# Kernel tuning notes

Measured on AMD Instinct MI355X. Metric: run time of the kernel, lower is better.

The kernel has to match this reference:

```python
import jax, jax.numpy as jnp
import numpy as np
from jax import lax

KERNEL_EPS = 1e-4   # eps in softmax_kernel
ATTN_EPS = 1e-6     # eps in causal_linear_attention
CHUNK = 64          # chunk length for the causal scan


def softmax_kernel(data, projection_matrix, is_query):
    # data: [b,h,n,d], projection_matrix: [r,d]
    d = data.shape[-1]
    r = projection_matrix.shape[0]
    data_normalizer = d ** -0.25
    ratio = r ** -0.5
    data_dash = jnp.einsum('bhnd,rd->bhnr', data_normalizer * data, projection_matrix)
    diag_data = (jnp.sum(data ** 2, axis=-1) * 0.5 * data_normalizer ** 2)[..., None]  # [b,h,n,1]
    if is_query:
        stab = jnp.max(data_dash, axis=-1, keepdims=True)
    else:
        stab = jnp.max(data_dash)
    return ratio * (jnp.exp(data_dash - diag_data - stab) + KERNEL_EPS)


def causal_linear_attention(qp, kp, v, chunk=CHUNK, eps=ATTN_EPS):
    # qp,kp: [b,h,n,r] feature maps; v: [b,h,n,e]
    b, h, n, r = qp.shape
    e = v.shape[-1]
    nc = n // chunk
    # -> [nc, b, h, chunk, *] for lax.scan over chunks
    qs = jnp.moveaxis(qp.reshape(b, h, nc, chunk, r), 2, 0)
    ks = jnp.moveaxis(kp.reshape(b, h, nc, chunk, r), 2, 0)
    vs = jnp.moveaxis(v.reshape(b, h, nc, chunk, e), 2, 0)

    def step(carry, xs):
        k_last, ctx_last = carry  # [b,h,r], [b,h,r,e]
        qch, kch, vch = xs        # [b,h,c,r], [b,h,c,r], [b,h,c,e]
        k_cum = k_last[:, :, None, :] + jnp.cumsum(kch, axis=2)              # [b,h,c,r]
        D_inv = 1.0 / jnp.einsum('bhcr,bhcr->bhc', qch, k_cum + eps)         # [b,h,c]
        ctx = jnp.einsum('bhcr,bhce->bhcre', kch, vch)                       # [b,h,c,r,e]
        ctx_cum = ctx_last[:, :, None] + jnp.cumsum(ctx, axis=2)             # [b,h,c,r,e]
        out = jnp.einsum('bhcre,bhcr,bhc->bhce', ctx_cum, qch, D_inv)        # [b,h,c,e]
        return (k_cum[:, :, -1], ctx_cum[:, :, -1]), out

    init = (jnp.zeros((b, h, r), qp.dtype), jnp.zeros((b, h, r, e), qp.dtype))
    _, outs = lax.scan(step, init, (qs, ks, vs))  # outs: [nc,b,h,c,e]
    return jnp.moveaxis(outs, 0, 2).reshape(b, h, n, e)


def setup_inputs() -> dict:
    key = jax.random.key(0)
    kq, kk, kv, kp = jax.random.split(key, 4)
    b, h, n, d, r = 2, 8, 4096, 64, 256
    q = jax.random.normal(kq, (b, h, n, d), dtype=jnp.float32)
    k = jax.random.normal(kk, (b, h, n, d), dtype=jnp.float32)
    v = jax.random.normal(kv, (b, h, n, d), dtype=jnp.float32)
    projection_matrix = jax.random.normal(kp, (r, d), dtype=jnp.float32)
    return {"q": q, "k": k, "v": v, "projection_matrix": projection_matrix}


def reference(q, k, v, projection_matrix):
    qp = softmax_kernel(q, projection_matrix, is_query=True)
    kp = softmax_kernel(k, projection_matrix, is_query=False)
    return causal_linear_attention(qp, kp, v)
```

## Files before the change

kernel.cpp:

```cpp
#include <hip/hip_runtime.h>


typedef unsigned short ushort_t;
typedef __attribute__((ext_vector_type(8))) short bf16x8;
typedef __attribute__((ext_vector_type(4))) float f32x4;

#define KEPS 1e-4f
#define AEPS 1e-6f
#define NORMIZER 0.35355339059327373f
#define RATIO 0.0625f

__device__ __forceinline__ ushort_t bf16r(float f) {
  unsigned u = __float_as_uint(f);
  return (ushort_t)((u + 0x7fffu + ((u >> 16) & 1u)) >> 16);
}
__device__ __forceinline__ float ubf(ushort_t h) {
  return __uint_as_float((unsigned)h << 16);
}
__device__ __forceinline__ unsigned cvtpk(float lo, float hi) {
  unsigned r;
  asm("v_cvt_pk_bf16_f32 %0, %1, %2" : "=v"(r) : "v"(lo), "v"(hi));
  return r;
}
union U32V { unsigned u[4]; bf16x8 v; };

__global__ __launch_bounds__(256) void pconv_kernel(
    const float* __restrict__ P, ushort_t* __restrict__ Phi,
    ushort_t* __restrict__ Plo)
{
  int idx = blockIdx.x * 1024 + threadIdx.x;
  #pragma unroll
  for (int p = 0; p < 4; ++p) {
    int i = idx + p * 256;
    float x = P[i];
    ushort_t h = bf16r(x);
    Phi[i] = h;
    Plo[i] = bf16r(x - ubf(h));
  }
}

__device__ __forceinline__ void stage_ptile(const ushort_t* __restrict__ gt,
                                            ushort_t* lds0, int tid) {
  int wv = tid >> 6, lane = tid & 63;
  #pragma unroll
  for (int i = 0; i < 2; ++i) {
    int D = i * 256 + wv * 64 + lane;
    int row = D >> 3, c3 = D & 7;
    int sc = (row << 3) | (c3 ^ (row & 7));
    __builtin_amdgcn_global_load_lds(
        (const __attribute__((address_space(1))) void*)(gt + sc * 8),
        (__attribute__((address_space(3))) void*)(lds0 + (i * 256 + wv * 64) * 8),
        16, 0, 0);
  }
}

__global__ __launch_bounds__(256, 4) void feat_mfma(
    const float* __restrict__ Q, const float* __restrict__ K,
    const float* __restrict__ V,
    const ushort_t* __restrict__ Phi, const ushort_t* __restrict__ Plo,
    ushort_t* __restrict__ qp, ushort_t* __restrict__ E,
    float* __restrict__ bmax,
    ushort_t* __restrict__ SE, float* __restrict__ zE,
    float* __restrict__ SV)
{
  __shared__ union {
    struct {
      ushort_t Xhi[64 * 72];
      ushort_t Xlo[64 * 72];
      ushort_t Pt[2][4096];
    } s;
    ushort_t outb[64 * 268];
    ushort_t Et[256 * 72];
  } u;
  __shared__ float diagS[64];
  __shared__ float redm[4];

  int bid = blockIdx.x, tid = threadIdx.x;
  bool isK = bid < 1024;
  int bc = bid;
  const float* X = isK ? K : Q;
  size_t rowbase = (size_t)(isK ? bid : bid - 1024) * 64;

  int lane = tid & 63, wv = tid >> 6;
  int n15 = lane & 15, quad = lane >> 4;

  stage_ptile(Phi, &u.s.Pt[0][0], tid);

  float vraw[16];
  if (isK) {
    #pragma unroll
    for (int ks = 0; ks < 2; ++ks)
      #pragma unroll
      for (int jj = 0; jj < 8; ++jj) {
        int pos = quad * 8 + 32 * ks + jj;
        vraw[ks * 8 + jj] = V[rowbase * 64 + (size_t)pos * 64 + 16 * wv + n15];
      }
  }

  #pragma unroll
  for (int p = 0; p < 4; ++p) {
    int idx = tid + p * 256;
    int row = idx >> 4, c4 = idx & 15;
    float4 x = *(const float4*)&X[(rowbase + row) * 64 + c4 * 4];
    unsigned h0 = cvtpk(x.x, x.y);
    unsigned h1 = cvtpk(x.z, x.w);
    float r0 = x.x - __uint_as_float(h0 << 16);
    float r1 = x.y - __uint_as_float(h0 & 0xffff0000u);
    float r2 = x.z - __uint_as_float(h1 << 16);
    float r3 = x.w - __uint_as_float(h1 & 0xffff0000u);
    unsigned l0 = cvtpk(r0, r1);
    unsigned l1 = cvtpk(r2, r3);
    unsigned* ph = (unsigned*)&u.s.Xhi[row * 72 + c4 * 4];
    ph[0] = h0; ph[1] = h1;
    unsigned* pl = (unsigned*)&u.s.Xlo[row * 72 + c4 * 4];
    pl[0] = l0; pl[1] = l1;
    float ss = x.x * x.x + x.y * x.y + x.z * x.z + x.w * x.w;
    ss += __shfl_xor(ss, 1, 64); ss += __shfl_xor(ss, 2, 64);
    ss += __shfl_xor(ss, 4, 64); ss += __shfl_xor(ss, 8, 64);
    if ((tid & 15) == 0) diagS[row] = 0.0625f * ss;
  }

  bf16x8 aV[2];
  if (isK) {
    float vsum = 0.f;
    #pragma unroll
    for (int ks = 0; ks < 2; ++ks) {
      U32V A;
      #pragma unroll
      for (int j2 = 0; j2 < 4; ++j2) {
        vsum += vraw[ks * 8 + 2 * j2] + vraw[ks * 8 + 2 * j2 + 1];
        A.u[j2] = cvtpk(vraw[ks * 8 + 2 * j2], vraw[ks * 8 + 2 * j2 + 1]);
      }
      aV[ks] = A.v;
    }
    vsum += __shfl_xor(vsum, 16, 64);
    vsum += __shfl_xor(vsum, 32, 64);
    if (quad == 0) SV[(size_t)bc * 64 + 16 * wv + n15] = vsum;
  }

  __syncthreads();

  bf16x8 ah[2], al[2];
  #pragma unroll
  for (int ks = 0; ks < 2; ++ks) {
    int off = (16 * wv + n15) * 72 + quad * 8 + 32 * ks;
    ah[ks] = *(const bf16x8*)&u.s.Xhi[off];
    al[ks] = *(const bf16x8*)&u.s.Xlo[off];
  }

  f32x4 acc[16];
  #pragma unroll
  for (int tc = 0; tc < 16; ++tc) acc[tc] = f32x4{0.f, 0.f, 0.f, 0.f};

  int buf = 0;
  #pragma unroll
  for (int t = 0; t < 8; ++t) {
    int q4 = t >> 1;
    bool isLo = t & 1;
    if (t) {
      asm volatile("s_waitcnt vmcnt(0)" ::: "memory");
      __builtin_amdgcn_s_barrier();
    }
    if (t < 7) {
      int tn = t + 1;
      const ushort_t* gt = ((tn & 1) ? Plo : Phi) + (size_t)(tn >> 1) * 4096;
      stage_ptile(gt, &u.s.Pt[buf ^ 1][0], tid);
    }
    #pragma unroll
    for (int tcl = 0; tcl < 4; ++tcl) {
      f32x4 a = acc[q4 * 4 + tcl];
      #pragma unroll
      for (int ks = 0; ks < 2; ++ks) {
        int jr = 16 * tcl + n15;
        int rc = (quad + 4 * ks) ^ (n15 & 7);
        bf16x8 b = *(const bf16x8*)&u.s.Pt[buf][jr * 64 + rc * 8];
        a = __builtin_amdgcn_mfma_f32_16x16x32_bf16(ah[ks], b, a, 0, 0, 0);
        if (!isLo)
          a = __builtin_amdgcn_mfma_f32_16x16x32_bf16(al[ks], b, a, 0, 0, 0);
      }
      acc[q4 * 4 + tcl] = a;
    }
    buf ^= 1;
  }

  float dg[4];
  #pragma unroll
  for (int r = 0; r < 4; ++r) dg[r] = diagS[16 * wv + quad * 4 + r];

  float sub[4];
  if (!isK) {
    #pragma unroll
    for (int r = 0; r < 4; ++r) {
      float mx = -3.0e38f;
      #pragma unroll
      for (int tc = 0; tc < 16; ++tc) mx = fmaxf(mx, acc[tc][r]);
      #pragma unroll
      for (int s = 1; s < 16; s <<= 1) mx = fmaxf(mx, __shfl_xor(mx, s, 64));
      sub[r] = dg[r] + NORMIZER * mx;
    }
  } else {
    float bm = -3.0e38f;
    #pragma unroll
    for (int tc = 0; tc < 16; ++tc)
      #pragma unroll
      for (int r = 0; r < 4; ++r) bm = fmaxf(bm, acc[tc][r]);
    #pragma unroll
    for (int s = 1; s < 64; s <<= 1) bm = fmaxf(bm, __shfl_xor(bm, s, 64));
    if (lane == 0) redm[wv] = bm;
    #pragma unroll
    for (int r = 0; r < 4; ++r) sub[r] = dg[r];
  }

  unsigned hp[16][2];
  __syncthreads();
  ushort_t* dst = (isK ? E : qp) + rowbase * 256;
  #pragma unroll
  for (int tc = 0; tc < 16; ++tc) {
    #pragma unroll
    for (int rp = 0; rp < 2; ++rp) {
      float e0 = __expf(NORMIZER * acc[tc][2 * rp]     - sub[2 * rp]);
      float e1 = __expf(NORMIZER * acc[tc][2 * rp + 1] - sub[2 * rp + 1]);
      float v0 = isK ? e0 : RATIO * (e0 + KEPS);
      float v1 = isK ? e1 : RATIO * (e1 + KEPS);
      unsigned pk = cvtpk(v0, v1);
      hp[tc][rp] = pk;
      int row = 16 * wv + quad * 4 + 2 * rp;
      u.outb[row * 268 + 16 * tc + n15] = (ushort_t)pk;
      u.outb[(row + 1) * 268 + 16 * tc + n15] = (ushort_t)(pk >> 16);
    }
  }
  __syncthreads();
  #pragma unroll
  for (int p = 0; p < 8; ++p) {
    int g = (tid + p * 256) * 8;
    int row = g >> 8, c0 = g & 255;
    bf16x8 v0 = *(const bf16x8*)&u.outb[row * 268 + c0];
    *(bf16x8*)&dst[row * 256 + c0] = v0;
  }

  if (isK && tid == 0) {
    float m4 = fmaxf(fmaxf(redm[0], redm[1]), fmaxf(redm[2], redm[3]));
    bmax[bc] = NORMIZER * m4;
  }

  if (!isK) return;

  __syncthreads();

  #pragma unroll
  for (int tc = 0; tc < 16; ++tc) {
    int j = 16 * tc + n15;
    int rot = 8 * ((j >> 3) & 7);
    int pw = (16 * wv + quad * 4 + rot) & 63;
    ushort4 w4;
    w4.x = (ushort_t)(hp[tc][0] & 0xffffu);
    w4.y = (ushort_t)(hp[tc][0] >> 16);
    w4.z = (ushort_t)(hp[tc][1] & 0xffffu);
    w4.w = (ushort_t)(hp[tc][1] >> 16);
    *(ushort4*)&u.Et[j * 72 + pw] = w4;
  }
  __syncthreads();

  {
    float s = 0.f;
    #pragma unroll
    for (int m8 = 0; m8 < 8; ++m8) {
      bf16x8 r8 = *(const bf16x8*)&u.Et[tid * 72 + m8 * 8];
      #pragma unroll
      for (int x = 0; x < 8; ++x) s += ubf((ushort_t)r8[x]);
    }
    zE[(size_t)bc * 256 + tid] = s;
  }

  f32x4 acc2[16];
  #pragma unroll
  for (int tc = 0; tc < 16; ++tc) {
    int j = 16 * tc + n15;
    int rot = 8 * ((j >> 3) & 7);
    f32x4 a = {0.f, 0.f, 0.f, 0.f};
    #pragma unroll
    for (int ks = 0; ks < 2; ++ks) {
      int pr = (quad * 8 + 32 * ks + rot) & 63;
      bf16x8 b = *(const bf16x8*)&u.Et[j * 72 + pr];
      a = __builtin_amdgcn_mfma_f32_16x16x32_bf16(aV[ks], b, a, 0, 0, 0);
    }
    acc2[tc] = a;
  }
  __syncthreads();

  #pragma unroll
  for (int tc = 0; tc < 16; ++tc)
    #pragma unroll
    for (int rp = 0; rp < 2; ++rp) {
      unsigned pk = cvtpk(acc2[tc][2 * rp], acc2[tc][2 * rp + 1]);
      int e0 = 16 * wv + quad * 4 + 2 * rp;
      u.outb[e0 * 268 + 16 * tc + n15] = (ushort_t)pk;
      u.outb[(e0 + 1) * 268 + 16 * tc + n15] = (ushort_t)(pk >> 16);
    }
  __syncthreads();
  ushort_t* sdst = SE + rowbase * 256;
  #pragma unroll
  for (int p = 0; p < 8; ++p) {
    int g = (tid + p * 256) * 8;
    int e = g >> 8, j0 = g & 255;
    bf16x8 v0 = *(const bf16x8*)&u.outb[e * 268 + j0];
    *(bf16x8*)&sdst[e * 256 + j0] = v0;
  }
}

__global__ __launch_bounds__(256) void prefix_kernel(
    ushort_t* __restrict__ S, float* __restrict__ zE,
    const float* __restrict__ SV, const float* __restrict__ bmax)
{
  __shared__ float redk[4];
  int tid = threadIdx.x;
  {
    float bm = fmaxf(fmaxf(bmax[tid], bmax[tid + 256]),
                     fmaxf(bmax[tid + 512], bmax[tid + 768]));
    #pragma unroll
    for (int s = 1; s < 64; s <<= 1) bm = fmaxf(bm, __shfl_xor(bm, s, 64));
    if ((tid & 63) == 0) redk[tid >> 6] = bm;
  }
  __syncthreads();
  float m = fmaxf(fmaxf(redk[0], redk[1]), fmaxf(redk[2], redk[3]));

  int b = blockIdx.x;
  float c1 = RATIO * __expf(-m);
  const float c0 = RATIO * KEPS;
  if (b < 1024) {
    int flat = b * 256 + tid;
    int bh = flat >> 14;
    int idx = flat & 16383;
    int e = idx >> 8;
    size_t base = (size_t)bh * 1048576 + idx;
    const float* svp = SV + (size_t)bh * 4096 + e;
    float runE = 0.f, runV = 0.f;
    for (int cc = 0; cc < 64; cc += 8) {
      ushort_t t[8]; float sv[8];
      #pragma unroll
      for (int u2 = 0; u2 < 8; ++u2) {
        t[u2] = S[base + (size_t)(cc + u2) * 16384];
        sv[u2] = svp[(size_t)(cc + u2) * 64];
      }
      #pragma unroll
      for (int u2 = 0; u2 < 8; ++u2) {
        S[base + (size_t)(cc + u2) * 16384] = bf16r(c1 * runE + c0 * runV);
        runE += ubf(t[u2]);
        runV += sv[u2];
      }
    }
  } else {
    int bh = b - 1024;
    int j = tid;
    size_t base = (size_t)bh * 16384 + j;
    float run = 0.f;
    for (int cc = 0; cc < 64; cc += 8) {
      float t[8];
      #pragma unroll
      for (int u2 = 0; u2 < 8; ++u2)
        t[u2] = zE[base + (size_t)(cc + u2) * 256];
      #pragma unroll
      for (int u2 = 0; u2 < 8; ++u2) {
        zE[base + (size_t)(cc + u2) * 256] = run;
        run += c1 * t[u2] + 64.0f * c0;
      }
    }
  }
}

__device__ __forceinline__ void stage_tile(const ushort_t* __restrict__ gt,
                                           ushort_t* lds0, int tid, int wv) {
  #pragma unroll
  for (int i = 0; i < 2; ++i) {
    int D = i * 256 + tid;
    int row = D >> 5, cl = D & 31;
    int sc = (row << 5) | (cl ^ (row & 7));
    __builtin_amdgcn_global_load_lds(
        (const __attribute__((address_space(1))) void*)(gt + sc * 8),
        (__attribute__((address_space(3))) void*)(lds0 + (i * 256 + wv * 64) * 8),
        16, 0, 0);
  }
}

__global__ __launch_bounds__(256) void fused_mfma(
    const ushort_t* __restrict__ qp, const ushort_t* __restrict__ E,
    const float* __restrict__ bmax, const float* __restrict__ Z,
    const ushort_t* __restrict__ S, const float* __restrict__ V,
    float* __restrict__ out)
{
  __shared__ ushort_t As[64 * 72];
  __shared__ ushort_t Vt[64 * 72];
  __shared__ ushort_t Bst[2][4096];
  __shared__ float zv[256];
  __shared__ float qsumS[64];
  __shared__ float dqS[64];
  __shared__ float redk[4];

  int bc = blockIdx.x, tid = threadIdx.x;
  int lane = tid & 63, wv = tid >> 6;
  int n15 = lane & 15, quad = lane >> 4;
  const float c0 = RATIO * KEPS;
  size_t base = (size_t)bc * 16384;

  {
    float bm = fmaxf(fmaxf(bmax[tid], bmax[tid + 256]),
                     fmaxf(bmax[tid + 512], bmax[tid + 768]));
    #pragma unroll
    for (int s = 1; s < 64; s <<= 1) bm = fmaxf(bm, __shfl_xor(bm, s, 64));
    if (lane == 0) redk[wv] = bm;
  }
  zv[tid] = Z[(size_t)bc * 256 + tid] + AEPS;
  #pragma unroll
  for (int p = 0; p < 16; ++p) {
    int idx = tid + p * 256;
    int t = idx >> 6, e = idx & 63;
    Vt[e * 72 + t] = bf16r(V[(size_t)bc * 4096 + idx]);
  }
  __syncthreads();
  float m = fmaxf(fmaxf(redk[0], redk[1]), fmaxf(redk[2], redk[3]));
  float c1 = RATIO * __expf(-m);

  stage_tile(E + base, &Bst[0][0], tid, wv);

  bf16x8 aQ[8];
  #pragma unroll
  for (int ks = 0; ks < 8; ++ks)
    aQ[ks] = *(const bf16x8*)&qp[base + (size_t)(16 * wv + n15) * 256 + quad * 8 + 32 * ks];

  float qsum = 0.f, dq = 0.f;
  #pragma unroll
  for (int ks = 0; ks < 8; ++ks)
    #pragma unroll
    for (int j = 0; j < 8; ++j) {
      float qv = ubf((ushort_t)aQ[ks][j]);
      qsum += qv;
      dq += qv * zv[quad * 8 + 32 * ks + j];
    }
  qsum += __shfl_xor(qsum, 16, 64); qsum += __shfl_xor(qsum, 32, 64);
  dq   += __shfl_xor(dq, 16, 64);   dq   += __shfl_xor(dq, 32, 64);
  if (quad == 0) { qsumS[16 * wv + n15] = qsum; dqS[16 * wv + n15] = dq; }

  float rs[4] = {0.f, 0.f, 0.f, 0.f};
  float dinv[4] = {0.f, 0.f, 0.f, 0.f};

  #pragma unroll
  for (int t = 0; t < 8; ++t) {
    asm volatile("s_waitcnt vmcnt(0)" ::: "memory");
    __builtin_amdgcn_s_barrier();
    if (t < 7) {
      const ushort_t* gt = (t < 3) ? (E + base + (size_t)(t + 1) * 4096)
                                   : (S + base + (size_t)(t - 3) * 4096);
      stage_tile(gt, &Bst[(t + 1) & 1][0], tid, wv);
    }

    bf16x8 bf[8];
    #pragma unroll
    for (int ks = 0; ks < 8; ++ks) {
      int rc = (4 * ks + quad) ^ (n15 & 7);
      bf[ks] = *(const bf16x8*)&Bst[t & 1][(n15 * 32 + rc) * 8];
    }
    f32x4 g = {0.f, 0.f, 0.f, 0.f};
    #pragma unroll
    for (int ks = 0; ks < 8; ++ks)
      g = __builtin_amdgcn_mfma_f32_16x16x32_bf16(aQ[ks], bf[ks], g, 0, 0, 0);

    if (t < 4) {
      int tc = t;
      #pragma unroll
      for (int rp = 0; rp < 2; ++rp) {
        int i0 = 16 * wv + quad * 4 + 2 * rp;
        int tt = 16 * tc + n15;
        float v0 = (tt <= i0)     ? (c1 * g[2 * rp]     + c0 * qsumS[i0])     : 0.f;
        float v1 = (tt <= i0 + 1) ? (c1 * g[2 * rp + 1] + c0 * qsumS[i0 + 1]) : 0.f;
        unsigned pk = cvtpk(v0, v1);
        As[i0 * 72 + tt] = (ushort_t)pk;
        As[(i0 + 1) * 72 + tt] = (ushort_t)(pk >> 16);
        rs[2 * rp] += v0;
        rs[2 * rp + 1] += v1;
      }
      if (t == 3) {
        #pragma unroll
        for (int r = 0; r < 4; ++r) {
          float v2 = rs[r];
          #pragma unroll
          for (int s = 1; s < 16; s <<= 1) v2 += __shfl_xor(v2, s, 64);
          int i = 16 * wv + quad * 4 + r;
          dinv[r] = 1.f / (dqS[i] + v2);
        }
      }
    } else {
      int ec = t - 4;
      f32x4 o = g;
      #pragma unroll
      for (int ks = 0; ks < 2; ++ks) {
        bf16x8 a2 = *(const bf16x8*)&As[(16 * wv + n15) * 72 + quad * 8 + 32 * ks];
        bf16x8 b2 = *(const bf16x8*)&Vt[(16 * ec + n15) * 72 + quad * 8 + 32 * ks];
        o = __builtin_amdgcn_mfma_f32_16x16x32_bf16(a2, b2, o, 0, 0, 0);
      }
      #pragma unroll
      for (int r = 0; r < 4; ++r) {
        int i = 16 * wv + quad * 4 + r;
        out[(size_t)bc * 4096 + (size_t)i * 64 + 16 * ec + n15] = o[r] * dinv[r];
      }
    }
  }
}

extern "C" void kernel_launch(void* const* d_in, const int* in_sizes, int n_in,
                              void* d_out, int out_size, void* d_ws, size_t ws_size,
                              hipStream_t stream)
{
  const float* q = (const float*)d_in[0];
  const float* k = (const float*)d_in[1];
  const float* v = (const float*)d_in[2];
  const float* P = (const float*)d_in[3];
  float* out = (float*)d_out;

  ushort_t* qp  = (ushort_t*)d_ws;
  ushort_t* E   = qp + 16777216;
  ushort_t* S   = E + 16777216;
  float*    zE  = (float*)(S + 16777216);
  float*    SV  = zE + 262144;
  ushort_t* Phi = (ushort_t*)(SV + 65536);
  ushort_t* Plo = Phi + 16384;
  float*    bmax = (float*)(Plo + 16384);

  pconv_kernel<<<16, 256, 0, stream>>>(P, Phi, Plo);
  feat_mfma<<<2048, 256, 0, stream>>>(q, k, v, Phi, Plo, qp, E, bmax,
                                      S, zE, SV);
  prefix_kernel<<<1040, 256, 0, stream>>>(S, zE, SV, bmax);
  fused_mfma<<<1024, 256, 0, stream>>>(qp, E, bmax, zE, S, v, out);
}
```

Baseline: 156.1 us.

## Fuse query feature-map computation into the attention kernel, dropping qp round trip

Query feature maps are no longer computed by feat_mfma blocks and written to a global qp buffer. fused_mfma now projects its own Q chunk with the bf16 hi/lo split MFMA, applies the per-row max stabilisation and exp in registers, and stages the result through LDS to build the A operands. This removes a 32 MB bf16 write plus read and halves the feat_mfma grid. In exchange fused_mfma gains more LDS use through a union, more registers and a longer serial prologue, which may lower occupancy in the critical attention kernel.

Measured after the change: 149.0 us. -4.5%, faster.

```diff
diff --git a/kernel.cpp b/kernel.cpp
--- a/kernel.cpp
+++ b/kernel.cpp
@@ -54,12 +54,24 @@
   }
 }
 
+__device__ __forceinline__ void stage_tile(const ushort_t* __restrict__ gt,
+                                           ushort_t* lds0, int tid, int wv) {
+  #pragma unroll
+  for (int i = 0; i < 2; ++i) {
+    int D = i * 256 + tid;
+    int row = D >> 5, cl = D & 31;
+    int sc = (row << 5) | (cl ^ (row & 7));
+    __builtin_amdgcn_global_load_lds(
+        (const __attribute__((address_space(1))) void*)(gt + sc * 8),
+        (__attribute__((address_space(3))) void*)(lds0 + (i * 256 + wv * 64) * 8),
+        16, 0, 0);
+  }
+}
+
 __global__ __launch_bounds__(256, 4) void feat_mfma(
-    const float* __restrict__ Q, const float* __restrict__ K,
-    const float* __restrict__ V,
+    const float* __restrict__ K, const float* __restrict__ V,
     const ushort_t* __restrict__ Phi, const ushort_t* __restrict__ Plo,
-    ushort_t* __restrict__ qp, ushort_t* __restrict__ E,
-    float* __restrict__ bmax,
+    ushort_t* __restrict__ E, float* __restrict__ bmax,
     ushort_t* __restrict__ SE, float* __restrict__ zE,
     float* __restrict__ SV)
 {
@@ -75,11 +87,8 @@
   __shared__ float diagS[64];
   __shared__ float redm[4];
 
-  int bid = blockIdx.x, tid = threadIdx.x;
-  bool isK = bid < 1024;
-  int bc = bid;
-  const float* X = isK ? K : Q;
-  size_t rowbase = (size_t)(isK ? bid : bid - 1024) * 64;
+  int bc = blockIdx.x, tid = threadIdx.x;
+  size_t rowbase = (size_t)bc * 64;
 
   int lane = tid & 63, wv = tid >> 6;
   int n15 = lane & 15, quad = lane >> 4;
@@ -87,21 +96,19 @@
   stage_ptile(Phi, &u.s.Pt[0][0], tid);
 
   float vraw[16];
-  if (isK) {
-    #pragma unroll
-    for (int ks = 0; ks < 2; ++ks)
-      #pragma unroll
-      for (int jj = 0; jj < 8; ++jj) {
-        int pos = quad * 8 + 32 * ks + jj;
-        vraw[ks * 8 + jj] = V[rowbase * 64 + (size_t)pos * 64 + 16 * wv + n15];
-      }
-  }
+  #pragma unroll
+  for (int ks = 0; ks < 2; ++ks)
+    #pragma unroll
+    for (int jj = 0; jj < 8; ++jj) {
+      int pos = quad * 8 + 32 * ks + jj;
+      vraw[ks * 8 + jj] = V[rowbase * 64 + (size_t)pos * 64 + 16 * wv + n15];
+    }
 
   #pragma unroll
   for (int p = 0; p < 4; ++p) {
     int idx = tid + p * 256;
     int row = idx >> 4, c4 = idx & 15;
-    float4 x = *(const float4*)&X[(rowbase + row) * 64 + c4 * 4];
+    float4 x = *(const float4*)&K[(rowbase + row) * 64 + c4 * 4];
     unsigned h0 = cvtpk(x.x, x.y);
     unsigned h1 = cvtpk(x.z, x.w);
     float r0 = x.x - __uint_as_float(h0 << 16);
@@ -121,7 +128,7 @@
   }
 
   bf16x8 aV[2];
-  if (isK) {
+  {
     float vsum = 0.f;
     #pragma unroll
     for (int ks = 0; ks < 2; ++ks) {
@@ -187,18 +194,7 @@
   #pragma unroll
   for (int r = 0; r < 4; ++r) dg[r] = diagS[16 * wv + quad * 4 + r];
 
-  float sub[4];
-  if (!isK) {
-    #pragma unroll
-    for (int r = 0; r < 4; ++r) {
-      float mx = -3.0e38f;
-      #pragma unroll
-      for (int tc = 0; tc < 16; ++tc) mx = fmaxf(mx, acc[tc][r]);
-      #pragma unroll
-      for (int s = 1; s < 16; s <<= 1) mx = fmaxf(mx, __shfl_xor(mx, s, 64));
-      sub[r] = dg[r] + NORMIZER * mx;
-    }
-  } else {
+  {
     float bm = -3.0e38f;
     #pragma unroll
     for (int tc = 0; tc < 16; ++tc)
@@ -207,22 +203,18 @@
     #pragma unroll
     for (int s = 1; s < 64; s <<= 1) bm = fmaxf(bm, __shfl_xor(bm, s, 64));
     if (lane == 0) redm[wv] = bm;
-    #pragma unroll
-    for (int r = 0; r < 4; ++r) sub[r] = dg[r];
   }
 
   unsigned hp[16][2];
   __syncthreads();
-  ushort_t* dst = (isK ? E : qp) + rowbase * 256;
+  ushort_t* dst = E + rowbase * 256;
   #pragma unroll
   for (int tc = 0; tc < 16; ++tc) {
     #pragma unroll
     for (int rp = 0; rp < 2; ++rp) {
-      float e0 = __expf(NORMIZER * acc[tc][2 * rp]     - sub[2 * rp]);
-      float e1 = __expf(NORMIZER * acc[tc][2 * rp + 1] - sub[2 * rp + 1]);
-      float v0 = isK ? e0 : RATIO * (e0 + KEPS);
-      float v1 = isK ? e1 : RATIO * (e1 + KEPS);
-      unsigned pk = cvtpk(v0, v1);
+      float e0 = __expf(NORMIZER * acc[tc][2 * rp]     - dg[2 * rp]);
+      float e1 = __expf(NORMIZER * acc[tc][2 * rp + 1] - dg[2 * rp + 1]);
+      unsigned pk = cvtpk(e0, e1);
       hp[tc][rp] = pk;
       int row = 16 * wv + quad * 4 + 2 * rp;
       u.outb[row * 268 + 16 * tc + n15] = (ushort_t)pk;
@@ -238,12 +230,10 @@
     *(bf16x8*)&dst[row * 256 + c0] = v0;
   }
 
-  if (isK && tid == 0) {
+  if (tid == 0) {
     float m4 = fmaxf(fmaxf(redm[0], redm[1]), fmaxf(redm[2], redm[3]));
     bmax[bc] = NORMIZER * m4;
   }
-
-  if (!isK) return;
 
   __syncthreads();
 
@@ -368,32 +358,23 @@
   }
 }
 
-__device__ __forceinline__ void stage_tile(const ushort_t* __restrict__ gt,
-                                           ushort_t* lds0, int tid, int wv) {
-  #pragma unroll
-  for (int i = 0; i < 2; ++i) {
-    int D = i * 256 + tid;
-    int row = D >> 5, cl = D & 31;
-    int sc = (row << 5) | (cl ^ (row & 7));
-    __builtin_amdgcn_global_load_lds(
-        (const __attribute__((address_space(1))) void*)(gt + sc * 8),
-        (__attribute__((address_space(3))) void*)(lds0 + (i * 256 + wv * 64) * 8),
-        16, 0, 0);
-  }
-}
-
-__global__ __launch_bounds__(256) void fused_mfma(
-    const ushort_t* __restrict__ qp, const ushort_t* __restrict__ E,
-    const float* __restrict__ bmax, const float* __restrict__ Z,
-    const ushort_t* __restrict__ S, const float* __restrict__ V,
-    float* __restrict__ out)
+__global__ __launch_bounds__(256, 4) void fused_mfma(
+    const float* __restrict__ Q,
+    const ushort_t* __restrict__ Phi, const ushort_t* __restrict__ Plo,
+    const ushort_t* __restrict__ E, const float* __restrict__ bmax,
+    const float* __restrict__ Z, const ushort_t* __restrict__ S,
+    const float* __restrict__ V, float* __restrict__ out)
 {
-  __shared__ ushort_t As[64 * 72];
-  __shared__ ushort_t Vt[64 * 72];
+  __shared__ union {
+    struct { ushort_t Xhi[64 * 72]; ushort_t Xlo[64 * 72]; } x;
+    ushort_t qpb[64 * 136];
+    struct { ushort_t As[64 * 72]; ushort_t Vt[64 * 72]; } c;
+  } u;
   __shared__ ushort_t Bst[2][4096];
   __shared__ float zv[256];
   __shared__ float qsumS[64];
   __shared__ float dqS[64];
+  __shared__ float diagS[64];
   __shared__ float redk[4];
 
   int bc = blockIdx.x, tid = threadIdx.x;
@@ -401,6 +382,9 @@
   int n15 = lane & 15, quad = lane >> 4;
   const float c0 = RATIO * KEPS;
   size_t base = (size_t)bc * 16384;
+  size_t rowbase = (size_t)bc * 64;
+
+  stage_ptile(Phi, &Bst[0][0], tid);
 
   {
     float bm = fmaxf(fmaxf(bmax[tid], bmax[tid + 256]),
@@ -410,35 +394,139 @@
     if (lane == 0) redk[wv] = bm;
   }
   zv[tid] = Z[(size_t)bc * 256 + tid] + AEPS;
+
+  #pragma unroll
+  for (int p = 0; p < 4; ++p) {
+    int idx = tid + p * 256;
+    int row = idx >> 4, c4 = idx & 15;
+    float4 x = *(const float4*)&Q[(rowbase + row) * 64 + c4 * 4];
+    unsigned h0 = cvtpk(x.x, x.y);
+    unsigned h1 = cvtpk(x.z, x.w);
+    float r0 = x.x - __uint_as_float(h0 << 16);
+    float r1 = x.y - __uint_as_float(h0 & 0xffff0000u);
+    float r2 = x.z - __uint_as_float(h1 << 16);
+    float r3 = x.w - __uint_as_float(h1 & 0xffff0000u);
+    unsigned l0 = cvtpk(r0, r1);
+    unsigned l1 = cvtpk(r2, r3);
+    unsigned* ph = (unsigned*)&u.x.Xhi[row * 72 + c4 * 4];
+    ph[0] = h0; ph[1] = h1;
+    unsigned* pl = (unsigned*)&u.x.Xlo[row * 72 + c4 * 4];
+    pl[0] = l0; pl[1] = l1;
+    float ss = x.x * x.x + x.y * x.y + x.z * x.z + x.w * x.w;
+    ss += __shfl_xor(ss, 1, 64); ss += __shfl_xor(ss, 2, 64);
+    ss += __shfl_xor(ss, 4, 64); ss += __shfl_xor(ss, 8, 64);
+    if ((tid & 15) == 0) diagS[row] = 0.0625f * ss;
+  }
+  __syncthreads();
+  float m = fmaxf(fmaxf(redk[0], redk[1]), fmaxf(redk[2], redk[3]));
+  float c1 = RATIO * __expf(-m);
+
+  bf16x8 ah[2], al[2];
+  #pragma unroll
+  for (int ks = 0; ks < 2; ++ks) {
+    int off = (16 * wv + n15) * 72 + quad * 8 + 32 * ks;
+    ah[ks] = *(const bf16x8*)&u.x.Xhi[off];
+    al[ks] = *(const bf16x8*)&u.x.Xlo[off];
+  }
+
+  f32x4 acc[16];
+  #pragma unroll
+  for (int tc = 0; tc < 16; ++tc) acc[tc] = f32x4{0.f, 0.f, 0.f, 0.f};
+
+  int buf = 0;
+  #pragma unroll
+  for (int t = 0; t < 8; ++t) {
+    int q4 = t >> 1;
+    bool isLo = t & 1;
+    if (t) {
+      asm volatile("s_waitcnt vmcnt(0)" ::: "memory");
+      __builtin_amdgcn_s_barrier();
+    }
+    if (t < 7) {
+      int tn = t + 1;
+      const ushort_t* gt = ((tn & 1) ? Plo : Phi) + (size_t)(tn >> 1) * 4096;
+      stage_ptile(gt, &Bst[buf ^ 1][0], tid);
+    } else {
+      stage_tile(E + base, &Bst[buf ^ 1][0], tid, wv);
+    }
+    #pragma unroll
+    for (int tcl = 0; tcl < 4; ++tcl) {
+      f32x4 a = acc[q4 * 4 + tcl];
+      #pragma unroll
+      for (int ks = 0; ks < 2; ++ks) {
+        int jr = 16 * tcl + n15;
+        int rc = (quad + 4 * ks) ^ (n15 & 7);
+        bf16x8 b = *(const bf16x8*)&Bst[buf][jr * 64 + rc * 8];
+        a = __builtin_amdgcn_mfma_f32_16x16x32_bf16(ah[ks], b, a, 0, 0, 0);
+        if (!isLo)
+          a = __builtin_amdgcn_mfma_f32_16x16x32_bf16(al[ks], b, a, 0, 0, 0);
+      }
+      acc[q4 * 4 + tcl] = a;
+    }
+    buf ^= 1;
+  }
+
+  float sub[4];
+  {
+    float dg[4];
+    #pragma unroll
+    for (int r = 0; r < 4; ++r) dg[r] = diagS[16 * wv + quad * 4 + r];
+    #pragma unroll
+    for (int r = 0; r < 4; ++r) {
+      float mx = -3.0e38f;
+      #pragma unroll
+      for (int tc = 0; tc < 16; ++tc) mx = fmaxf(mx, acc[tc][r]);
+      #pragma unroll
+      for (int s = 1; s < 16; s <<= 1) mx = fmaxf(mx, __shfl_xor(mx, s, 64));
+      sub[r] = dg[r] + NORMIZER * mx;
+    }
+  }
+
+  float qsum = 0.f, dq = 0.f;
+  bf16x8 aQ[8];
+  #pragma unroll
+  for (int h = 0; h < 2; ++h) {
+    if (h) __syncthreads();
+    #pragma unroll
+    for (int tcl = 0; tcl < 8; ++tcl) {
+      int tc = 8 * h + tcl;
+      #pragma unroll
+      for (int rp = 0; rp < 2; ++rp) {
+        float e0 = __expf(NORMIZER * acc[tc][2 * rp]     - sub[2 * rp]);
+        float e1 = __expf(NORMIZER * acc[tc][2 * rp + 1] - sub[2 * rp + 1]);
+        unsigned pk = cvtpk(RATIO * (e0 + KEPS), RATIO * (e1 + KEPS));
+        int i0 = 16 * wv + quad * 4 + 2 * rp;
+        int cp = 16 * tcl + n15;
+        u.qpb[i0 * 136 + cp] = (ushort_t)pk;
+        u.qpb[(i0 + 1) * 136 + cp] = (ushort_t)(pk >> 16);
+      }
+    }
+    __syncthreads();
+    #pragma unroll
+    for (int ksl = 0; ksl < 4; ++ksl) {
+      int ks = 4 * h + ksl;
+      bf16x8 a = *(const bf16x8*)&u.qpb[(16 * wv + n15) * 136 + quad * 8 + 32 * ksl];
+      aQ[ks] = a;
+      #pragma unroll
+      for (int j = 0; j < 8; ++j) {
+        float qv = ubf((ushort_t)a[j]);
+        qsum += qv;
+        dq += qv * zv[quad * 8 + 32 * ks + j];
+      }
+    }
+  }
+  qsum += __shfl_xor(qsum, 16, 64); qsum += __shfl_xor(qsum, 32, 64);
+  dq   += __shfl_xor(dq, 16, 64);   dq   += __shfl_xor(dq, 32, 64);
+  if (quad == 0) { qsumS[16 * wv + n15] = qsum; dqS[16 * wv + n15] = dq; }
+
+  __syncthreads();
+
   #pragma unroll
   for (int p = 0; p < 16; ++p) {
     int idx = tid + p * 256;
     int t = idx >> 6, e = idx & 63;
-    Vt[e * 72 + t] = bf16r(V[(size_t)bc * 4096 + idx]);
-  }
-  __syncthreads();
-  float m = fmaxf(fmaxf(redk[0], redk[1]), fmaxf(redk[2], redk[3]));
-  float c1 = RATIO * __expf(-m);
-
-  stage_tile(E + base, &Bst[0][0], tid, wv);
-
-  bf16x8 aQ[8];
-  #pragma unroll
-  for (int ks = 0; ks < 8; ++ks)
-    aQ[ks] = *(const bf16x8*)&qp[base + (size_t)(16 * wv + n15) * 256 + quad * 8 + 32 * ks];
-
-  float qsum = 0.f, dq = 0.f;
-  #pragma unroll
-  for (int ks = 0; ks < 8; ++ks)
-    #pragma unroll
-    for (int j = 0; j < 8; ++j) {
-      float qv = ubf((ushort_t)aQ[ks][j]);
-      qsum += qv;
-      dq += qv * zv[quad * 8 + 32 * ks + j];
-    }
-  qsum += __shfl_xor(qsum, 16, 64); qsum += __shfl_xor(qsum, 32, 64);
-  dq   += __shfl_xor(dq, 16, 64);   dq   += __shfl_xor(dq, 32, 64);
-  if (quad == 0) { qsumS[16 * wv + n15] = qsum; dqS[16 * wv + n15] = dq; }
+    u.c.Vt[e * 72 + t] = bf16r(V[(size_t)bc * 4096 + idx]);
+  }
 
   float rs[4] = {0.f, 0.f, 0.f, 0.f};
   float dinv[4] = {0.f, 0.f, 0.f, 0.f};
@@ -473,8 +561,8 @@
         float v0 = (tt <= i0)     ? (c1 * g[2 * rp]     + c0 * qsumS[i0])     : 0.f;
         float v1 = (tt <= i0 + 1) ? (c1 * g[2 * rp + 1] + c0 * qsumS[i0 + 1]) : 0.f;
         unsigned pk = cvtpk(v0, v1);
-        As[i0 * 72 + tt] = (ushort_t)pk;
-        As[(i0 + 1) * 72 + tt] = (ushort_t)(pk >> 16);
+        u.c.As[i0 * 72 + tt] = (ushort_t)pk;
+        u.c.As[(i0 + 1) * 72 + tt] = (ushort_t)(pk >> 16);
         rs[2 * rp] += v0;
         rs[2 * rp + 1] += v1;
       }
@@ -493,8 +581,8 @@
       f32x4 o = g;
       #pragma unroll
       for (int ks = 0; ks < 2; ++ks) {
-        bf16x8 a2 = *(const bf16x8*)&As[(16 * wv + n15) * 72 + quad * 8 + 32 * ks];
-        bf16x8 b2 = *(const bf16x8*)&Vt[(16 * ec + n15) * 72 + quad * 8 + 32 * ks];
+        bf16x8 a2 = *(const bf16x8*)&u.c.As[(16 * wv + n15) * 72 + quad * 8 + 32 * ks];
+        bf16x8 b2 = *(const bf16x8*)&u.c.Vt[(16 * ec + n15) * 72 + quad * 8 + 32 * ks];
         o = __builtin_amdgcn_mfma_f32_16x16x32_bf16(a2, b2, o, 0, 0, 0);
       }
       #pragma unroll
@@ -516,8 +604,7 @@
   const float* P = (const float*)d_in[3];
   float* out = (float*)d_out;
 
-  ushort_t* qp  = (ushort_t*)d_ws;
-  ushort_t* E   = qp + 16777216;
+  ushort_t* E   = (ushort_t*)d_ws;
   ushort_t* S   = E + 16777216;
   float*    zE  = (float*)(S + 16777216);
   float*    SV  = zE + 262144;
@@ -526,8 +613,7 @@
   float*    bmax = (float*)(Plo + 16384);
 
   pconv_kernel<<<16, 256, 0, stream>>>(P, Phi, Plo);
-  feat_mfma<<<2048, 256, 0, stream>>>(q, k, v, Phi, Plo, qp, E, bmax,
-                                      S, zE, SV);
+  feat_mfma<<<1024, 256, 0, stream>>>(k, v, Phi, Plo, E, bmax, S, zE, SV);
   prefix_kernel<<<1040, 256, 0, stream>>>(S, zE, SV, bmax);
-  fused_mfma<<<1024, 256, 0, stream>>>(qp, E, bmax, zE, S, v, out);
-}
+  fused_mfma<<<1024, 256, 0, stream>>>(q, Phi, Plo, E, bmax, zE, S, v, out);
+}
```
